# Optimization experiments

Measured on AMD Instinct MI355X. Metric: run time of the kernel, lower is better.

The kernel has to match this reference:

```python
import jax, jax.numpy as jnp
import numpy as np

TIME_UNITS = 10.0
EPS_LN = 1e-5
N_NODES, N_EDGES, BATCH, T_IN = 20000, 320000, 8, 12
H_PROB, H_VEL = 64, 32


def _layernorm(x, g, b):
    mu = jnp.mean(x, axis=-1, keepdims=True)
    var = jnp.mean((x - mu) ** 2, axis=-1, keepdims=True)
    return (x - mu) / jnp.sqrt(var + EPS_LN) * g + b


def setup_inputs() -> dict:
    key = jax.random.key(0)
    ks = jax.random.split(key, 20)
    s = 0.1
    inp = {}
    inp['upstream'] = jax.random.uniform(ks[0], (N_EDGES, BATCH, T_IN), jnp.float32)
    inp['downstream'] = jax.random.uniform(ks[1], (N_EDGES, BATCH, T_IN), jnp.float32)
    inp['feature'] = jax.random.uniform(ks[2], (N_NODES, BATCH, T_IN), jnp.float32)
    inp['distance'] = jax.random.uniform(ks[3], (N_EDGES,), jnp.float32, 10.0, 500.0)
    inp['src'] = jax.random.randint(ks[4], (N_EDGES,), 0, N_NODES, jnp.int32)
    inp['dst'] = jax.random.randint(ks[5], (N_EDGES,), 0, N_NODES, jnp.int32)
    inp['fc_w'] = jax.random.normal(ks[6], (H_PROB, T_IN), jnp.float32) * s
    inp['attn_w'] = jax.random.normal(ks[7], (1, 2 * H_PROB + 1), jnp.float32) * s
    inp['ln2_g'] = jnp.ones((2 * H_PROB + 1,), jnp.float32)
    inp['ln2_b'] = jnp.zeros((2 * H_PROB + 1,), jnp.float32)
    inp['v11_w'] = jax.random.normal(ks[8], (H_VEL, T_IN), jnp.float32) * s
    inp['v11_b'] = jnp.zeros((H_VEL,), jnp.float32)
    inp['ln11_g'] = jnp.ones((H_VEL,), jnp.float32)
    inp['ln11_b'] = jnp.zeros((H_VEL,), jnp.float32)
    inp['v12_w'] = jax.random.normal(ks[9], (1, H_VEL), jnp.float32) * s
    inp['v12_b'] = jnp.zeros((1,), jnp.float32)
    inp['v21_w'] = jax.random.normal(ks[10], (H_VEL, T_IN), jnp.float32) * s
    inp['v21_b'] = jnp.zeros((H_VEL,), jnp.float32)
    inp['ln21_g'] = jnp.ones((H_VEL,), jnp.float32)
    inp['ln21_b'] = jnp.zeros((H_VEL,), jnp.float32)
    inp['v22_w'] = jax.random.normal(ks[11], (1, H_VEL), jnp.float32) * s
    inp['v22_b'] = jnp.zeros((1,), jnp.float32)
    inp['v3_w'] = jax.random.normal(ks[12], (1, 2), jnp.float32) * s
    inp['v3_b'] = jnp.zeros((1,), jnp.float32)
    inp['alpha'] = jnp.ones((N_EDGES, 1), jnp.float32)
    return inp


def reference(upstream, downstream, feature, distance, src, dst,
              fc_w, attn_w, ln2_g, ln2_b,
              v11_w, v11_b, ln11_g, ln11_b, v12_w, v12_b,
              v21_w, v21_b, ln21_g, ln21_b, v22_w, v22_b,
              v3_w, v3_b, alpha):
    N, B, T = feature.shape
    Tf = jnp.asarray(T, feature.dtype)

    # --- Velocity_Model_NAM (eval mode: dropout = identity) ---
    def branch(x, w1, b1, g, bn, w2, b2):
        h = jax.nn.relu(_layernorm(x @ w1.T + b1, g, bn))
        return jax.nn.sigmoid(h @ w2.T + b2)  # [E,B,1]

    xu = branch(upstream, v11_w, v11_b, ln11_g, ln11_b, v12_w, v12_b)
    xd = branch(downstream, v21_w, v21_b, ln21_g, ln21_b, v22_w, v22_b)
    v = jnp.log1p(jnp.exp((jnp.concatenate([xu, xd], -1) @ v3_w.T + v3_b)[..., 0]))  # [E,B]

    # --- per-edge travel time and diffusion kernel ---
    Tt = distance[:, None] / (v + 1e-5)                # [E,B]
    T_idx = jnp.round(Tt / TIME_UNITS)
    T_idx = jnp.where(T_idx < 0, 0.0, T_idx)
    T_idx = jnp.where(T_idx > Tf, Tf - 1.0, T_idx)     # strictly > T_in, as in masked_fill
    F = 1.0 / (1.0 + alpha * Tt)                       # [E,B]
    n = jnp.maximum(Tf - T_idx, 1.0)                   # sequence length per (edge,batch)
    t = jnp.arange(T, dtype=feature.dtype)
    mask = t < n[..., None]
    expo = jnp.maximum(n[..., None] - 1.0 - t, 0.0)    # decreasing exponents n-1..0
    diffusion = jnp.where(mask, F[..., None] * jnp.power(1.0 - F[..., None], expo), 0.0)  # [E,B,T]

    # --- Probabilistic_Model: embeddings + edge softmax normalized per SOURCE node ---
    z = feature @ fc_w.T                               # [N,B,64]
    zc = jnp.concatenate([z[src], z[dst], jax.lax.stop_gradient(v)[..., None]], -1)  # [E,B,129]
    a = jax.nn.leaky_relu((_layernorm(zc, ln2_g, ln2_b) @ attn_w.T)[..., 0], 0.01)   # [E,B]
    m = jax.ops.segment_max(a, src, num_segments=N)
    ex = jnp.exp(a - m[src])
    den = jax.ops.segment_sum(ex, src, num_segments=N)
    score = ex / den[src]

    # --- mailbox reduce: attention-weighted diffusion prediction per destination ---
    pred_edge = jnp.sum(diffusion * feature[src], -1)  # [E,B]
    pred = jax.ops.segment_sum(score * pred_edge, dst, num_segments=N)  # [N,B]
    return pred
```

## Files before the change

kernel.cpp:

```cpp
#include <hip/hip_runtime.h>
#include <math.h>

#define TB 8
#define TT 12
#define HV 32

typedef float v2f __attribute__((ext_vector_type(2)));

#define PK_B1 384
#define PK_TL 416
#define PK_STRIDE 576

__device__ __forceinline__ float vel_branch32(const v2f xv[6], const float* swb, float b2) {
  v2f h2[16];
  v2f s1v = {0.f, 0.f}, s2v = {0.f, 0.f};
#pragma unroll
  for (int jp = 0; jp < 16; ++jp) {
    const float4* wr = (const float4*)(swb + jp * 24);
    float4 a0 = wr[0], a1 = wr[1], a2 = wr[2];
    float4 c0 = wr[3], c1 = wr[4], c2 = wr[5];
    v2f bj = *(const v2f*)(swb + PK_B1 + 2*jp);
    v2f p0 = xv[0] * (v2f){a0.x, a0.y};
    p0 = __builtin_elementwise_fma(xv[1], (v2f){a0.z, a0.w}, p0);
    p0 = __builtin_elementwise_fma(xv[2], (v2f){a1.x, a1.y}, p0);
    p0 = __builtin_elementwise_fma(xv[3], (v2f){a1.z, a1.w}, p0);
    p0 = __builtin_elementwise_fma(xv[4], (v2f){a2.x, a2.y}, p0);
    p0 = __builtin_elementwise_fma(xv[5], (v2f){a2.z, a2.w}, p0);
    v2f p1 = xv[0] * (v2f){c0.x, c0.y};
    p1 = __builtin_elementwise_fma(xv[1], (v2f){c0.z, c0.w}, p1);
    p1 = __builtin_elementwise_fma(xv[2], (v2f){c1.x, c1.y}, p1);
    p1 = __builtin_elementwise_fma(xv[3], (v2f){c1.z, c1.w}, p1);
    p1 = __builtin_elementwise_fma(xv[4], (v2f){c2.x, c2.y}, p1);
    p1 = __builtin_elementwise_fma(xv[5], (v2f){c2.z, c2.w}, p1);
    v2f hv = { p0.x + p0.y + bj.x, p1.x + p1.y + bj.y };
    h2[jp] = hv;
    s1v += hv;
    s2v = __builtin_elementwise_fma(hv, hv, s2v);
  }
  float s1 = s1v.x + s1v.y;
  float s2 = s2v.x + s2v.y;
  float mu  = s1 * (1.f/HV);
  float var = s2 * (1.f/HV) - mu*mu;
  float inv = 1.f / sqrtf(var + 1e-5f);
  v2f mu2  = {mu, mu};
  v2f inv2 = {inv, inv};
  v2f zero = {0.f, 0.f};
  v2f acc2 = {b2, 0.f};
#pragma unroll
  for (int jp = 0; jp < 16; ++jp) {
    float4 t0 = *(const float4*)(swb + PK_TL + 8*jp);
    v2f w2v   = *(const v2f*)(swb + PK_TL + 8*jp + 4);
    v2f gv  = {t0.x, t0.y};
    v2f bnv = {t0.z, t0.w};
    v2f yl = __builtin_elementwise_fma((h2[jp] - mu2) * inv2, gv, bnv);
    yl = __builtin_elementwise_max(yl, zero);
    acc2 = __builtin_elementwise_fma(yl, w2v, acc2);
  }
  return 1.f / (1.f + __expf(-(acc2.x + acc2.y)));
}

__device__ double vel_branch64(const float* x,
    const float* __restrict__ w1, const float* __restrict__ b1,
    const float* __restrict__ g,  const float* __restrict__ bn,
    const float* __restrict__ w2, float b2) {
  double s1 = 0.0, s2 = 0.0;
  for (int j = 0; j < HV; ++j) {
    double hj = (double)b1[j];
    for (int t = 0; t < TT; ++t) hj = fma((double)x[t], (double)w1[j*TT+t], hj);
    s1 += hj;
    s2 = fma(hj, hj, s2);
  }
  double mu  = s1 / (double)HV;
  double var = s2 / (double)HV - mu*mu;
  double inv = 1.0 / sqrt(var + 1e-5);
  double acc = (double)b2;
  for (int j = 0; j < HV; ++j) {
    double hj = (double)b1[j];
    for (int t = 0; t < TT; ++t) hj = fma((double)x[t], (double)w1[j*TT+t], hj);
    double yl = (hj - mu) * inv * (double)g[j] + (double)bn[j];
    if (yl < 0.0) yl = 0.0;
    acc = fma(yl, (double)w2[j], acc);
  }
  return 1.0 / (1.0 + exp(-acc));
}

__global__ void __launch_bounds__(256) k_prep(
    float* __restrict__ den, float* __restrict__ pred, int nb,
    const float* __restrict__ attn_w, const float* __restrict__ ln2_g,
    const float* __restrict__ ln2_b,
    const float* __restrict__ v11_w, const float* __restrict__ v11_b,
    const float* __restrict__ ln11_g, const float* __restrict__ ln11_b,
    const float* __restrict__ v12_w, const float* __restrict__ v12_b,
    const float* __restrict__ v21_w, const float* __restrict__ v21_b,
    const float* __restrict__ ln21_g, const float* __restrict__ ln21_b,
    const float* __restrict__ v22_w, const float* __restrict__ v22_b,
    const float* __restrict__ v3_w, const float* __restrict__ v3_b,
    float* __restrict__ scal, float* __restrict__ pack, int* __restrict__ fixcnt) {
  int idx = blockIdx.x * blockDim.x + threadIdx.x;
  for (int i = idx; i < nb; i += gridDim.x * blockDim.x) { den[i] = 0.f; pred[i] = 0.f; }
  if (blockIdx.x == 0) {
    __shared__ float sg[256], sb[256];
    float a = 0.f, b = 0.f;
    if (threadIdx.x < 129) {
      float w = attn_w[threadIdx.x];
      a = w * ln2_g[threadIdx.x];
      b = w * ln2_b[threadIdx.x];
    }
    sg[threadIdx.x] = a; sb[threadIdx.x] = b;
    __syncthreads();
    for (int s = 128; s > 0; s >>= 1) {
      if (threadIdx.x < s) { sg[threadIdx.x] += sg[threadIdx.x+s]; sb[threadIdx.x] += sb[threadIdx.x+s]; }
      __syncthreads();
    }
    if (threadIdx.x == 0) {
      scal[0] = sg[0]; scal[1] = sb[0];
      scal[2] = attn_w[128] * ln2_g[128];
      scal[3] = v12_b[0];  scal[4] = v22_b[0];
      scal[5] = v3_w[0];   scal[6] = v3_w[1];  scal[7] = v3_b[0];
      fixcnt[0] = 0;
    }
  } else if (blockIdx.x <= 2) {
    int br = blockIdx.x - 1;
    const float* W1 = br ? v21_w : v11_w;
    const float* B1 = br ? v21_b : v11_b;
    const float* G  = br ? ln21_g : ln11_g;
    const float* BN = br ? ln21_b : ln11_b;
    const float* W2 = br ? v22_w : v12_w;
    float* p = pack + br * PK_STRIDE;
    for (int i = threadIdx.x; i < PK_STRIDE; i += 256) {
      float val = 0.f;
      if (i < PK_B1)      val = W1[i];
      else if (i < PK_TL) val = B1[i - PK_B1];
      else if (i < 544) {
        int q = i - PK_TL, jp = q >> 3, k = q & 7;
        int j = 2*jp + (k & 1);
        if (k < 2)      val = G[j];
        else if (k < 4) val = BN[j];
        else if (k < 6) val = W2[j];
      }
      p[i] = val;
    }
  }
}

__global__ void __launch_bounds__(256, 2) k_node(
    const float* __restrict__ feature, const float* __restrict__ fc_w,
    const float* __restrict__ attn_w,  const float* __restrict__ ln2_g,
    float4* __restrict__ nodepre, int n_nodes) {
  int idx = blockIdx.x * blockDim.x + threadIdx.x;
  int total = n_nodes * TB;
  if (idx >= total) return;
  const float4* f4 = (const float4*)(feature + (size_t)idx * TT);
  float4 fa = f4[0], fb = f4[1], fcv = f4[2];
  v2f xv[6] = {{fa.x,fa.y},{fa.z,fa.w},{fb.x,fb.y},{fb.z,fb.w},{fcv.x,fcv.y},{fcv.z,fcv.w}};
  float q = 0.f, r = 0.f, ps = 0.f, pd = 0.f;
#pragma unroll 8
  for (int i = 0; i < 64; ++i) {
    v2f p = {0.f, 0.f};
#pragma unroll
    for (int k = 0; k < 6; ++k)
      p = __builtin_elementwise_fma(xv[k], *(const v2f*)(fc_w + i*TT + 2*k), p);
    float z = p.x + p.y;
    q += z;
    r  = fmaf(z, z, r);
    ps = fmaf(z, attn_w[i]      * ln2_g[i],      ps);
    pd = fmaf(z, attn_w[64 + i] * ln2_g[64 + i], pd);
  }
  nodepre[idx] = make_float4(q, r, ps, pd);
}

__global__ void __launch_bounds__(256, 2) k_edge1(
    const float* __restrict__ upstream, const float* __restrict__ downstream,
    const float* __restrict__ feature,  const float* __restrict__ distance,
    const int* __restrict__ src, const int* __restrict__ dst,
    const float* __restrict__ alpha,
    const float* __restrict__ pack,
    const float4* __restrict__ nodepre, const float* __restrict__ scal,
    float2* __restrict__ epbuf, float* __restrict__ den,
    int* __restrict__ fixcnt, int* __restrict__ fixlist, int fixcap,
    int n_edges) {
  __shared__ float sw[2 * PK_STRIDE];
  for (int i = threadIdx.x; i < 2 * PK_STRIDE / 4; i += 256)
    ((float4*)sw)[i] = ((const float4*)pack)[i];
  __syncthreads();

  int idx = blockIdx.x * blockDim.x + threadIdx.x;
  if (idx >= n_edges * TB) return;
  int e = idx >> 3, b = idx & 7;

  float sc0 = scal[0], sc1 = scal[1], aw128 = scal[2];
  float b2u = scal[3], b2d = scal[4];
  float w3a = scal[5], w3b = scal[6], b3 = scal[7];

  int s = src[e], d = dst[e];
  float dist = distance[e];
  float al   = alpha[e];
  const float4* f4 = (const float4*)(feature + ((size_t)s * TB + b) * TT);
  float4 f0 = f4[0], f1 = f4[1], f2 = f4[2];
  float4 nps = nodepre[(size_t)s * TB + b];
  float4 npd = nodepre[(size_t)d * TB + b];

  float xu, xd;
  {
    const float4* u4 = (const float4*)(upstream + (size_t)idx * TT);
    float4 a0 = u4[0], a1 = u4[1], a2 = u4[2];
    v2f xv[6] = {{a0.x,a0.y},{a0.z,a0.w},{a1.x,a1.y},{a1.z,a1.w},{a2.x,a2.y},{a2.z,a2.w}};
    xu = vel_branch32(xv, sw, b2u);
  }
  {
    const float4* d4 = (const float4*)(downstream + (size_t)idx * TT);
    float4 c0 = d4[0], c1 = d4[1], c2 = d4[2];
    v2f xv[6] = {{c0.x,c0.y},{c0.z,c0.w},{c1.x,c1.y},{c1.z,c1.w},{c2.x,c2.y},{c2.z,c2.w}};
    xd = vel_branch32(xv, sw + PK_STRIDE, b2d);
  }
  float y = fmaf(xu, w3a, fmaf(xd, w3b, b3));
  float v = fmaxf(y, 0.f) + __logf(1.f + __expf(-fabsf(y)));

  float tt  = dist / (v + 1e-5f);
  float th  = tt * 0.1f;
  float tif = rintf(th);

  float frac = th - tif;
  if (fabsf(fabsf(frac) - 0.5f) < 2.5e-4f && th < 11.0f) {
    int p = atomicAdd(fixcnt, 1);
    if (p < fixcap) fixlist[p] = idx;
  }

  int ti = (int)tif;
  ti = ti < 0 ? 0 : (ti > TT ? TT - 1 : ti);
  int n = TT - ti; n = n < 1 ? 1 : n;

  float F  = 1.f / fmaf(al, tt, 1.f);
  float om = 1.f - F;

  float feat[TT] = {f0.x,f0.y,f0.z,f0.w, f1.x,f1.y,f1.z,f1.w, f2.x,f2.y,f2.z,f2.w};
  float acc = 0.f;
#pragma unroll
  for (int t = 0; t < TT; ++t) {
    acc = (t < n) ? fmaf(acc, om, feat[t]) : acc;
  }
  float pe = F * acc;

  float sum   = nps.x + npd.x + v;
  float sumsq = nps.y + npd.y + v*v;
  float mu  = sum * (1.f/129.f);
  float var = sumsq * (1.f/129.f) - mu*mu;
  float S1  = nps.z + npd.w + v * aw128;
  float aa  = (S1 - mu*sc0) / sqrtf(var + 1e-5f) + sc1;
  float a   = aa >= 0.f ? aa : 0.01f*aa;
  float ex  = __expf(a);

  epbuf[idx] = make_float2(ex, pe);
  atomicAdd(&den[s * TB + b], ex);
}

__global__ void __launch_bounds__(256) k_fix(
    const float* __restrict__ upstream, const float* __restrict__ downstream,
    const float* __restrict__ feature,  const float* __restrict__ distance,
    const int* __restrict__ src, const int* __restrict__ dst,
    const float* __restrict__ v11_w, const float* __restrict__ v11_b,
    const float* __restrict__ ln11_g, const float* __restrict__ ln11_b,
    const float* __restrict__ v12_w, const float* __restrict__ v12_b,
    const float* __restrict__ v21_w, const float* __restrict__ v21_b,
    const float* __restrict__ ln21_g, const float* __restrict__ ln21_b,
    const float* __restrict__ v22_w, const float* __restrict__ v22_b,
    const float* __restrict__ v3_w, const float* __restrict__ v3_b,
    const float* __restrict__ alpha,
    const float4* __restrict__ nodepre, const float* __restrict__ scal,
    float2* __restrict__ epbuf, float* __restrict__ den,
    const int* __restrict__ fixcnt, const int* __restrict__ fixlist, int fixcap) {
  int cnt = fixcnt[0];
  if (cnt > fixcap) cnt = fixcap;
  int stride = gridDim.x * blockDim.x;
  for (int i = blockIdx.x * blockDim.x + threadIdx.x; i < cnt; i += stride) {
    int idx = fixlist[i];
    int e = idx >> 3, b = idx & 7;
    int s = src[e], d = dst[e];
    float dist = distance[e];
    float al   = alpha[e];

    const float* xr_u = upstream   + (size_t)idx * TT;
    const float* xr_d = downstream + (size_t)idx * TT;
    double xu64 = vel_branch64(xr_u, v11_w, v11_b, ln11_g, ln11_b, v12_w, v12_b[0]);
    double xd64 = vel_branch64(xr_d, v21_w, v21_b, ln21_g, ln21_b, v22_w, v22_b[0]);
    double y64  = xu64*(double)v3_w[0] + xd64*(double)v3_w[1] + (double)v3_b[0];
    double v64  = log1p(exp(y64));
    double tt64 = (double)dist / (v64 + 1e-5);
    float v   = (float)v64;
    float tt  = (float)tt64;
    float tif = (float)rint(tt64 * 0.1);

    int ti = (int)tif;
    ti = ti < 0 ? 0 : (ti > TT ? TT - 1 : ti);
    int n = TT - ti; n = n < 1 ? 1 : n;

    float F  = 1.f / fmaf(al, tt, 1.f);
    float om = 1.f - F;

    const float* feat = feature + ((size_t)s * TB + b) * TT;
    float acc = 0.f;
    for (int t = 0; t < n; ++t) acc = fmaf(acc, om, feat[t]);
    float pe = F * acc;

    float4 nps = nodepre[(size_t)s * TB + b];
    float4 npd = nodepre[(size_t)d * TB + b];
    float sum   = nps.x + npd.x + v;
    float sumsq = nps.y + npd.y + v*v;
    float mu  = sum * (1.f/129.f);
    float var = sumsq * (1.f/129.f) - mu*mu;
    float S1  = nps.z + npd.w + v * scal[2];
    float aa  = (S1 - mu*scal[0]) / sqrtf(var + 1e-5f) + scal[1];
    float a   = aa >= 0.f ? aa : 0.01f*aa;
    float ex  = __expf(a);

    float2 old = epbuf[idx];
    epbuf[idx] = make_float2(ex, pe);
    atomicAdd(&den[s * TB + b], ex - old.x);
  }
}

__global__ void __launch_bounds__(256) k_edge2(
    const int* __restrict__ src, const int* __restrict__ dst,
    const float2* __restrict__ epbuf,
    const float* __restrict__ den, float* __restrict__ pred, int n_edges) {
  int idx = blockIdx.x * blockDim.x + threadIdx.x;
  if (idx >= n_edges * TB) return;
  int e = idx >> 3, b = idx & 7;
  float2 ep = epbuf[idx];
  float score = ep.x / den[src[e] * TB + b];
  atomicAdd(&pred[dst[e] * TB + b], score * ep.y);
}

extern "C" void kernel_launch(void* const* d_in, const int* in_sizes, int n_in,
                              void* d_out, int out_size, void* d_ws, size_t ws_size,
                              hipStream_t stream) {
  const float* upstream   = (const float*)d_in[0];
  const float* downstream = (const float*)d_in[1];
  const float* feature    = (const float*)d_in[2];
  const float* distance   = (const float*)d_in[3];
  const int*   src        = (const int*)d_in[4];
  const int*   dst        = (const int*)d_in[5];
  const float* fc_w   = (const float*)d_in[6];
  const float* attn_w = (const float*)d_in[7];
  const float* ln2_g  = (const float*)d_in[8];
  const float* ln2_b  = (const float*)d_in[9];
  const float* v11_w  = (const float*)d_in[10];
  const float* v11_b  = (const float*)d_in[11];
  const float* ln11_g = (const float*)d_in[12];
  const float* ln11_b = (const float*)d_in[13];
  const float* v12_w  = (const float*)d_in[14];
  const float* v12_b  = (const float*)d_in[15];
  const float* v21_w  = (const float*)d_in[16];
  const float* v21_b  = (const float*)d_in[17];
  const float* ln21_g = (const float*)d_in[18];
  const float* ln21_b = (const float*)d_in[19];
  const float* v22_w  = (const float*)d_in[20];
  const float* v22_b  = (const float*)d_in[21];
  const float* v3_w   = (const float*)d_in[22];
  const float* v3_b   = (const float*)d_in[23];
  const float* alpha  = (const float*)d_in[24];

  int E  = in_sizes[4];
  int N  = in_sizes[2] / (TB * TT);
  int NB = N * TB;
  int EB = E * TB;
  int fixcap = EB / 8;

  float*  ws      = (float*)d_ws;
  float4* nodepre = (float4*)ws;
  float2* epbuf   = (float2*)(ws + 4 * (size_t)NB);
  float*  den     = ws + 4 * (size_t)NB + 2 * (size_t)EB;
  float*  scal    = den + NB;
  float*  pack    = scal + 8;
  int*    fixcnt  = (int*)(pack + 2 * PK_STRIDE);
  int*    fixlist = fixcnt + 4;
  float*  pred    = (float*)d_out;

  int blk = 256;
  k_prep<<<(NB + blk - 1) / blk, blk, 0, stream>>>(
      den, pred, NB, attn_w, ln2_g, ln2_b,
      v11_w, v11_b, ln11_g, ln11_b, v12_w, v12_b,
      v21_w, v21_b, ln21_g, ln21_b, v22_w, v22_b,
      v3_w, v3_b, scal, pack, fixcnt);
  k_node<<<(NB + blk - 1) / blk, blk, 0, stream>>>(feature, fc_w, attn_w, ln2_g, nodepre, N);
  k_edge1<<<(EB + blk - 1) / blk, blk, 0, stream>>>(
      upstream, downstream, feature, distance, src, dst, alpha,
      pack, nodepre, scal, epbuf, den, fixcnt, fixlist, fixcap, E);
  k_fix<<<16, blk, 0, stream>>>(
      upstream, downstream, feature, distance, src, dst,
      v11_w, v11_b, ln11_g, ln11_b, v12_w, v12_b,
      v21_w, v21_b, ln21_g, ln21_b, v22_w, v22_b,
      v3_w, v3_b, alpha,
      nodepre, scal, epbuf, den, fixcnt, fixlist, fixcap);
  k_edge2<<<(EB + blk - 1) / blk, blk, 0, stream>>>(src, dst, epbuf, den, pred, E);
}
```

Before: 171.0 us.

## Fuse prep into node kernel, stage fc_w in LDS, vectorize edge2 by pairs

Merges the k_prep initialization kernel into k_node, removing one launch. The node kernel now stages fc_w and the precomputed attn_w*ln2_g products in shared memory and reads them as float4. k_edge2 handles two batch entries per thread with vector loads of epbuf and den, and issues two atomics per thread. There is a possible ordering risk: block 0 writes scal and pack while other blocks run, though these are only consumed by later kernels.

```diff
diff --git a/kernel.cpp b/kernel.cpp
--- a/kernel.cpp
+++ b/kernel.cpp
@@ -84,9 +84,9 @@
   return 1.0 / (1.0 + exp(-acc));
 }
 
-__global__ void __launch_bounds__(256) k_prep(
-    float* __restrict__ den, float* __restrict__ pred, int nb,
-    const float* __restrict__ attn_w, const float* __restrict__ ln2_g,
+__global__ void __launch_bounds__(256, 2) k_node(
+    const float* __restrict__ feature, const float* __restrict__ fc_w,
+    const float* __restrict__ attn_w,  const float* __restrict__ ln2_g,
     const float* __restrict__ ln2_b,
     const float* __restrict__ v11_w, const float* __restrict__ v11_b,
     const float* __restrict__ ln11_g, const float* __restrict__ ln11_b,
@@ -95,9 +95,21 @@
     const float* __restrict__ ln21_g, const float* __restrict__ ln21_b,
     const float* __restrict__ v22_w, const float* __restrict__ v22_b,
     const float* __restrict__ v3_w, const float* __restrict__ v3_b,
-    float* __restrict__ scal, float* __restrict__ pack, int* __restrict__ fixcnt) {
+    float4* __restrict__ nodepre, float* __restrict__ den, float* __restrict__ pred,
+    float* __restrict__ scal, float* __restrict__ pack, int* __restrict__ fixcnt,
+    int nb) {
+  __shared__ float sfc[768];
+  __shared__ float saw[128];
+  for (int i = threadIdx.x; i < 768; i += 256) sfc[i] = fc_w[i];
+  if (threadIdx.x < 64) {
+    saw[2*threadIdx.x]     = attn_w[threadIdx.x]      * ln2_g[threadIdx.x];
+    saw[2*threadIdx.x + 1] = attn_w[64 + threadIdx.x] * ln2_g[64 + threadIdx.x];
+  }
+  __syncthreads();
+
   int idx = blockIdx.x * blockDim.x + threadIdx.x;
-  for (int i = idx; i < nb; i += gridDim.x * blockDim.x) { den[i] = 0.f; pred[i] = 0.f; }
+  if (idx < nb) { den[idx] = 0.f; pred[idx] = 0.f; }
+
   if (blockIdx.x == 0) {
     __shared__ float sg[256], sb[256];
     float a = 0.f, b = 0.f;
@@ -141,30 +153,28 @@
       p[i] = val;
     }
   }
-}
-
-__global__ void __launch_bounds__(256, 2) k_node(
-    const float* __restrict__ feature, const float* __restrict__ fc_w,
-    const float* __restrict__ attn_w,  const float* __restrict__ ln2_g,
-    float4* __restrict__ nodepre, int n_nodes) {
-  int idx = blockIdx.x * blockDim.x + threadIdx.x;
-  int total = n_nodes * TB;
-  if (idx >= total) return;
+
+  if (idx >= nb) return;
   const float4* f4 = (const float4*)(feature + (size_t)idx * TT);
   float4 fa = f4[0], fb = f4[1], fcv = f4[2];
   v2f xv[6] = {{fa.x,fa.y},{fa.z,fa.w},{fb.x,fb.y},{fb.z,fb.w},{fcv.x,fcv.y},{fcv.z,fcv.w}};
   float q = 0.f, r = 0.f, ps = 0.f, pd = 0.f;
-#pragma unroll 8
+#pragma unroll 4
   for (int i = 0; i < 64; ++i) {
-    v2f p = {0.f, 0.f};
-#pragma unroll
-    for (int k = 0; k < 6; ++k)
-      p = __builtin_elementwise_fma(xv[k], *(const v2f*)(fc_w + i*TT + 2*k), p);
+    const float4* row = (const float4*)(sfc + i * TT);
+    float4 w0 = row[0], w1 = row[1], w2 = row[2];
+    v2f p = xv[0] * (v2f){w0.x, w0.y};
+    p = __builtin_elementwise_fma(xv[1], (v2f){w0.z, w0.w}, p);
+    p = __builtin_elementwise_fma(xv[2], (v2f){w1.x, w1.y}, p);
+    p = __builtin_elementwise_fma(xv[3], (v2f){w1.z, w1.w}, p);
+    p = __builtin_elementwise_fma(xv[4], (v2f){w2.x, w2.y}, p);
+    p = __builtin_elementwise_fma(xv[5], (v2f){w2.z, w2.w}, p);
     float z = p.x + p.y;
+    v2f aw = *(const v2f*)(saw + 2*i);
     q += z;
     r  = fmaf(z, z, r);
-    ps = fmaf(z, attn_w[i]      * ln2_g[i],      ps);
-    pd = fmaf(z, attn_w[64 + i] * ln2_g[64 + i], pd);
+    ps = fmaf(z, aw.x, ps);
+    pd = fmaf(z, aw.y, pd);
   }
   nodepre[idx] = make_float4(q, r, ps, pd);
 }
@@ -322,13 +332,16 @@
 __global__ void __launch_bounds__(256) k_edge2(
     const int* __restrict__ src, const int* __restrict__ dst,
     const float2* __restrict__ epbuf,
-    const float* __restrict__ den, float* __restrict__ pred, int n_edges) {
+    const float* __restrict__ den, float* __restrict__ pred, int n_pairs) {
   int idx = blockIdx.x * blockDim.x + threadIdx.x;
-  if (idx >= n_edges * TB) return;
-  int e = idx >> 3, b = idx & 7;
-  float2 ep = epbuf[idx];
-  float score = ep.x / den[src[e] * TB + b];
-  atomicAdd(&pred[dst[e] * TB + b], score * ep.y);
+  if (idx >= n_pairs) return;
+  int row0 = idx * 2;
+  int e = row0 >> 3, b0 = row0 & 7;
+  float4 ep = ((const float4*)epbuf)[idx];
+  int s = src[e], d = dst[e];
+  float2 dn = *(const float2*)(den + s * TB + b0);
+  atomicAdd(&pred[d * TB + b0],     (ep.x / dn.x) * ep.y);
+  atomicAdd(&pred[d * TB + b0 + 1], (ep.z / dn.y) * ep.w);
 }
 
 extern "C" void kernel_launch(void* const* d_in, const int* in_sizes, int n_in,
@@ -377,12 +390,12 @@
   float*  pred    = (float*)d_out;
 
   int blk = 256;
-  k_prep<<<(NB + blk - 1) / blk, blk, 0, stream>>>(
-      den, pred, NB, attn_w, ln2_g, ln2_b,
+  k_node<<<(NB + blk - 1) / blk, blk, 0, stream>>>(
+      feature, fc_w, attn_w, ln2_g, ln2_b,
       v11_w, v11_b, ln11_g, ln11_b, v12_w, v12_b,
       v21_w, v21_b, ln21_g, ln21_b, v22_w, v22_b,
-      v3_w, v3_b, scal, pack, fixcnt);
-  k_node<<<(NB + blk - 1) / blk, blk, 0, stream>>>(feature, fc_w, attn_w, ln2_g, nodepre, N);
+      v3_w, v3_b,
+      nodepre, den, pred, scal, pack, fixcnt, NB);
   k_edge1<<<(EB + blk - 1) / blk, blk, 0, stream>>>(
       upstream, downstream, feature, distance, src, dst, alpha,
       pack, nodepre, scal, epbuf, den, fixcnt, fixlist, fixcap, E);
@@ -392,5 +405,5 @@
       v21_w, v21_b, ln21_g, ln21_b, v22_w, v22_b,
       v3_w, v3_b, alpha,
       nodepre, scal, epbuf, den, fixcnt, fixlist, fixcap);
-  k_edge2<<<(EB + blk - 1) / blk, blk, 0, stream>>>(src, dst, epbuf, den, pred, E);
-}
+  k_edge2<<<(EB / 2 + blk - 1) / blk, blk, 0, stream>>>(src, dst, epbuf, den, pred, EB / 2);
+}
```

Measured after the change: 183.9 us. +7.5%, slower.

## Split edge kernel into velocity kernel and gather/attention edge kernel

Applied to the files above, without the earlier changes.

The fused edge kernel is split in two. k_vel computes only the velocity MLP and writes v to a new per-edge buffer. k_fixv recomputes flagged entries in double precision, and a separate k_edge then does the gathers, diffusion, attention logit and denominator atomics. This separates the compute-heavy MLP from the gather-heavy scatter so each kernel can use registers and occupancy differently, and it simplifies the fix pass. The cost is an extra launch plus a write and re-read of the v buffer and distance.

```diff
diff --git a/kernel.cpp b/kernel.cpp
--- a/kernel.cpp
+++ b/kernel.cpp
@@ -169,14 +169,11 @@
   nodepre[idx] = make_float4(q, r, ps, pd);
 }
 
-__global__ void __launch_bounds__(256, 2) k_edge1(
+__global__ void __launch_bounds__(256, 2) k_vel(
     const float* __restrict__ upstream, const float* __restrict__ downstream,
-    const float* __restrict__ feature,  const float* __restrict__ distance,
-    const int* __restrict__ src, const int* __restrict__ dst,
-    const float* __restrict__ alpha,
-    const float* __restrict__ pack,
-    const float4* __restrict__ nodepre, const float* __restrict__ scal,
-    float2* __restrict__ epbuf, float* __restrict__ den,
+    const float* __restrict__ distance,
+    const float* __restrict__ pack, const float* __restrict__ scal,
+    float* __restrict__ vbuf,
     int* __restrict__ fixcnt, int* __restrict__ fixlist, int fixcap,
     int n_edges) {
   __shared__ float sw[2 * PK_STRIDE];
@@ -186,19 +183,11 @@
 
   int idx = blockIdx.x * blockDim.x + threadIdx.x;
   if (idx >= n_edges * TB) return;
-  int e = idx >> 3, b = idx & 7;
-
-  float sc0 = scal[0], sc1 = scal[1], aw128 = scal[2];
+  int e = idx >> 3;
+
   float b2u = scal[3], b2d = scal[4];
   float w3a = scal[5], w3b = scal[6], b3 = scal[7];
-
-  int s = src[e], d = dst[e];
   float dist = distance[e];
-  float al   = alpha[e];
-  const float4* f4 = (const float4*)(feature + ((size_t)s * TB + b) * TT);
-  float4 f0 = f4[0], f1 = f4[1], f2 = f4[2];
-  float4 nps = nodepre[(size_t)s * TB + b];
-  float4 npd = nodepre[(size_t)d * TB + b];
 
   float xu, xd;
   {
@@ -216,16 +205,66 @@
   float y = fmaf(xu, w3a, fmaf(xd, w3b, b3));
   float v = fmaxf(y, 0.f) + __logf(1.f + __expf(-fabsf(y)));
 
-  float tt  = dist / (v + 1e-5f);
-  float th  = tt * 0.1f;
-  float tif = rintf(th);
-
-  float frac = th - tif;
+  float th  = (dist / (v + 1e-5f)) * 0.1f;
+  float frac = th - rintf(th);
   if (fabsf(fabsf(frac) - 0.5f) < 2.5e-4f && th < 11.0f) {
     int p = atomicAdd(fixcnt, 1);
     if (p < fixcap) fixlist[p] = idx;
   }
 
+  vbuf[idx] = v;
+}
+
+__global__ void __launch_bounds__(256) k_fixv(
+    const float* __restrict__ upstream, const float* __restrict__ downstream,
+    const float* __restrict__ v11_w, const float* __restrict__ v11_b,
+    const float* __restrict__ ln11_g, const float* __restrict__ ln11_b,
+    const float* __restrict__ v12_w, const float* __restrict__ v12_b,
+    const float* __restrict__ v21_w, const float* __restrict__ v21_b,
+    const float* __restrict__ ln21_g, const float* __restrict__ ln21_b,
+    const float* __restrict__ v22_w, const float* __restrict__ v22_b,
+    const float* __restrict__ v3_w, const float* __restrict__ v3_b,
+    float* __restrict__ vbuf,
+    const int* __restrict__ fixcnt, const int* __restrict__ fixlist, int fixcap) {
+  int cnt = fixcnt[0];
+  if (cnt > fixcap) cnt = fixcap;
+  int stride = gridDim.x * blockDim.x;
+  for (int i = blockIdx.x * blockDim.x + threadIdx.x; i < cnt; i += stride) {
+    int idx = fixlist[i];
+    const float* xr_u = upstream   + (size_t)idx * TT;
+    const float* xr_d = downstream + (size_t)idx * TT;
+    double xu64 = vel_branch64(xr_u, v11_w, v11_b, ln11_g, ln11_b, v12_w, v12_b[0]);
+    double xd64 = vel_branch64(xr_d, v21_w, v21_b, ln21_g, ln21_b, v22_w, v22_b[0]);
+    double y64  = xu64*(double)v3_w[0] + xd64*(double)v3_w[1] + (double)v3_b[0];
+    double v64  = log1p(exp(y64));
+    vbuf[idx] = (float)v64;
+  }
+}
+
+__global__ void __launch_bounds__(256) k_edge(
+    const float* __restrict__ feature, const float* __restrict__ distance,
+    const int* __restrict__ src, const int* __restrict__ dst,
+    const float* __restrict__ alpha,
+    const float4* __restrict__ nodepre, const float* __restrict__ scal,
+    const float* __restrict__ vbuf,
+    float2* __restrict__ epbuf, float* __restrict__ den,
+    int n_edges) {
+  int idx = blockIdx.x * blockDim.x + threadIdx.x;
+  if (idx >= n_edges * TB) return;
+  int e = idx >> 3, b = idx & 7;
+
+  int s = src[e], d = dst[e];
+  float dist = distance[e];
+  float al   = alpha[e];
+  float v    = vbuf[idx];
+  const float4* f4 = (const float4*)(feature + ((size_t)s * TB + b) * TT);
+  float4 f0 = f4[0], f1 = f4[1], f2 = f4[2];
+  float4 nps = nodepre[(size_t)s * TB + b];
+  float4 npd = nodepre[(size_t)d * TB + b];
+  float sc0 = scal[0], sc1 = scal[1], aw128 = scal[2];
+
+  float tt  = dist / (v + 1e-5f);
+  float tif = rintf(tt * 0.1f);
   int ti = (int)tif;
   ti = ti < 0 ? 0 : (ti > TT ? TT - 1 : ti);
   int n = TT - ti; n = n < 1 ? 1 : n;
@@ -252,71 +291,6 @@
 
   epbuf[idx] = make_float2(ex, pe);
   atomicAdd(&den[s * TB + b], ex);
-}
-
-__global__ void __launch_bounds__(256) k_fix(
-    const float* __restrict__ upstream, const float* __restrict__ downstream,
-    const float* __restrict__ feature,  const float* __restrict__ distance,
-    const int* __restrict__ src, const int* __restrict__ dst,
-    const float* __restrict__ v11_w, const float* __restrict__ v11_b,
-    const float* __restrict__ ln11_g, const float* __restrict__ ln11_b,
-    const float* __restrict__ v12_w, const float* __restrict__ v12_b,
-    const float* __restrict__ v21_w, const float* __restrict__ v21_b,
-    const float* __restrict__ ln21_g, const float* __restrict__ ln21_b,
-    const float* __restrict__ v22_w, const float* __restrict__ v22_b,
-    const float* __restrict__ v3_w, const float* __restrict__ v3_b,
-    const float* __restrict__ alpha,
-    const float4* __restrict__ nodepre, const float* __restrict__ scal,
-    float2* __restrict__ epbuf, float* __restrict__ den,
-    const int* __restrict__ fixcnt, const int* __restrict__ fixlist, int fixcap) {
-  int cnt = fixcnt[0];
-  if (cnt > fixcap) cnt = fixcap;
-  int stride = gridDim.x * blockDim.x;
-  for (int i = blockIdx.x * blockDim.x + threadIdx.x; i < cnt; i += stride) {
-    int idx = fixlist[i];
-    int e = idx >> 3, b = idx & 7;
-    int s = src[e], d = dst[e];
-    float dist = distance[e];
-    float al   = alpha[e];
-
-    const float* xr_u = upstream   + (size_t)idx * TT;
-    const float* xr_d = downstream + (size_t)idx * TT;
-    double xu64 = vel_branch64(xr_u, v11_w, v11_b, ln11_g, ln11_b, v12_w, v12_b[0]);
-    double xd64 = vel_branch64(xr_d, v21_w, v21_b, ln21_g, ln21_b, v22_w, v22_b[0]);
-    double y64  = xu64*(double)v3_w[0] + xd64*(double)v3_w[1] + (double)v3_b[0];
-    double v64  = log1p(exp(y64));
-    double tt64 = (double)dist / (v64 + 1e-5);
-    float v   = (float)v64;
-    float tt  = (float)tt64;
-    float tif = (float)rint(tt64 * 0.1);
-
-    int ti = (int)tif;
-    ti = ti < 0 ? 0 : (ti > TT ? TT - 1 : ti);
-    int n = TT - ti; n = n < 1 ? 1 : n;
-
-    float F  = 1.f / fmaf(al, tt, 1.f);
-    float om = 1.f - F;
-
-    const float* feat = feature + ((size_t)s * TB + b) * TT;
-    float acc = 0.f;
-    for (int t = 0; t < n; ++t) acc = fmaf(acc, om, feat[t]);
-    float pe = F * acc;
-
-    float4 nps = nodepre[(size_t)s * TB + b];
-    float4 npd = nodepre[(size_t)d * TB + b];
-    float sum   = nps.x + npd.x + v;
-    float sumsq = nps.y + npd.y + v*v;
-    float mu  = sum * (1.f/129.f);
-    float var = sumsq * (1.f/129.f) - mu*mu;
-    float S1  = nps.z + npd.w + v * scal[2];
-    float aa  = (S1 - mu*scal[0]) / sqrtf(var + 1e-5f) + scal[1];
-    float a   = aa >= 0.f ? aa : 0.01f*aa;
-    float ex  = __expf(a);
-
-    float2 old = epbuf[idx];
-    epbuf[idx] = make_float2(ex, pe);
-    atomicAdd(&den[s * TB + b], ex - old.x);
-  }
 }
 
 __global__ void __launch_bounds__(256) k_edge2(
@@ -374,6 +348,7 @@
   float*  pack    = scal + 8;
   int*    fixcnt  = (int*)(pack + 2 * PK_STRIDE);
   int*    fixlist = fixcnt + 4;
+  float*  vbuf    = (float*)(fixlist + fixcap);
   float*  pred    = (float*)d_out;
 
   int blk = 256;
@@ -383,14 +358,16 @@
       v21_w, v21_b, ln21_g, ln21_b, v22_w, v22_b,
       v3_w, v3_b, scal, pack, fixcnt);
   k_node<<<(NB + blk - 1) / blk, blk, 0, stream>>>(feature, fc_w, attn_w, ln2_g, nodepre, N);
-  k_edge1<<<(EB + blk - 1) / blk, blk, 0, stream>>>(
-      upstream, downstream, feature, distance, src, dst, alpha,
-      pack, nodepre, scal, epbuf, den, fixcnt, fixlist, fixcap, E);
-  k_fix<<<16, blk, 0, stream>>>(
-      upstream, downstream, feature, distance, src, dst,
+  k_vel<<<(EB + blk - 1) / blk, blk, 0, stream>>>(
+      upstream, downstream, distance, pack, scal,
+      vbuf, fixcnt, fixlist, fixcap, E);
+  k_fixv<<<16, blk, 0, stream>>>(
+      upstream, downstream,
       v11_w, v11_b, ln11_g, ln11_b, v12_w, v12_b,
       v21_w, v21_b, ln21_g, ln21_b, v22_w, v22_b,
-      v3_w, v3_b, alpha,
-      nodepre, scal, epbuf, den, fixcnt, fixlist, fixcap);
+      v3_w, v3_b, vbuf, fixcnt, fixlist, fixcap);
+  k_edge<<<(EB + blk - 1) / blk, blk, 0, stream>>>(
+      feature, distance, src, dst, alpha,
+      nodepre, scal, vbuf, epbuf, den, E);
   k_edge2<<<(EB + blk - 1) / blk, blk, 0, stream>>>(src, dst, epbuf, den, pred, E);
 }
```

New measurement: 192.3 us. 1.12x slower.
